# Optimization experiments

Measured on AMD Instinct MI355X. Metric: run time of the kernel, lower is better.

Reference implementation:

```python
import jax, jax.numpy as jnp
import numpy as np

B, T, F, H = 32, 8192, 256, 128


def setup_inputs() -> dict:
    key = jax.random.key(0)
    k1, k2, k3, k4, k5 = jax.random.split(key, 5)
    return {
        "encoder_outputs": jax.random.normal(k1, (B, T, F), dtype=jnp.float32),
        "dec_output": jax.random.normal(k2, (B, F), dtype=jnp.float32),
        "W1": jax.random.normal(k3, (F, H), dtype=jnp.float32) * 0.05,
        "W2": jax.random.normal(k4, (F, H), dtype=jnp.float32) * 0.05,
        "V": jax.random.normal(k5, (H, 1), dtype=jnp.float32) * 0.05,
    }


def reference(encoder_outputs, dec_output, W1, W2, V):
    # w1_e: [B,T,H]; w2_d: [B,1,H] (constant across timesteps, no real recurrence)
    w1_e = jnp.einsum("btf,fh->bth", encoder_outputs, W1)
    w2_d = (dec_output @ W2)[:, None, :]
    # scores[b,t] = V . tanh(W1 e_t + W2 d)  -> [B, T] (raw logits, no softmax in original call)
    scores = jnp.einsum("bth,h->bt", jnp.tanh(w1_e + w2_d), V[:, 0])
    return scores
```

## Files before the change

kernel.cpp:

```cpp
#include <hip/hip_runtime.h>

#define B_ 32
#define T_ 8192
#define F_ 256
#define H_ 128

typedef short bf16x8 __attribute__((ext_vector_type(8)));
typedef float f32x4  __attribute__((ext_vector_type(4)));

static __device__ __forceinline__ unsigned int pack_bf2(float lo, float hi) {
    unsigned int r;
    asm("v_cvt_pk_bf16_f32 %0, %1, %2" : "=v"(r) : "v"(lo), "v"(hi));
    return r;
}

static __device__ __forceinline__ float fast_tanh(float x) {
    float e = __builtin_amdgcn_exp2f(x * 2.8853900817779268f);
    return 1.f - 2.f * __builtin_amdgcn_rcpf(e + 1.f);
}

__global__ __launch_bounds__(256) void prep_kernel(const float* __restrict__ dec,
                                                   const float* __restrict__ W1,
                                                   const float* __restrict__ W2,
                                                   float* __restrict__ w2d,
                                                   uint4* __restrict__ frags) {
    const int blk = blockIdx.x, tid = threadIdx.x;
    if (blk < 32) {
        if (tid < H_) {
            const float* dp = dec + blk * F_;
            float s = 0.f;
            #pragma unroll 8
            for (int f = 0; f < F_; ++f) s += dp[f] * W2[f * H_ + tid];
            w2d[blk * H_ + tid] = s;
        }
    } else {
        const int e = (blk - 32) * 256 + tid;
        const int lane = e & 63;
        const int ks   = (e >> 6) & 7;
        const int nt   = e >> 9;
        const int q = lane >> 4, c = lane & 15;
        const int h = nt * 16 + c;
        const float* src = W1 + (q * 64 + ks * 8) * H_ + h;
        unsigned int u[4];
        #pragma unroll
        for (int jj = 0; jj < 4; ++jj) {
            float a = src[(2 * jj) * H_];
            float b = src[(2 * jj + 1) * H_];
            u[jj] = pack_bf2(a, b);
        }
        frags[e] = uint4{u[0], u[1], u[2], u[3]};
    }
}

__global__ __launch_bounds__(256) void attn_main(const float* __restrict__ enc,
                                                 const float* __restrict__ Vvec,
                                                 const float* __restrict__ w2d,
                                                 const uint4* __restrict__ frags,
                                                 float* __restrict__ out) {
    __shared__ __align__(16) unsigned char tile_lds[2][32 * 512];
    __shared__ float red[4][256];

    const int tid  = threadIdx.x;
    const int blk  = blockIdx.x;
    const int b    = blk >> 5;
    const int t0   = (blk & 31) << 8;
    const int w    = tid >> 6;
    const int lane = tid & 63;
    const int q    = lane >> 4;
    const int c    = lane & 15;

    bf16x8 bw[2][8];
    #pragma unroll
    for (int ntl = 0; ntl < 2; ++ntl)
        #pragma unroll
        for (int ks = 0; ks < 8; ++ks) {
            uint4 u = frags[((2 * w + ntl) * 8 + ks) * 64 + lane];
            bw[ntl][ks] = __builtin_bit_cast(bf16x8, u);
        }

    float Vv[2], wd[2];
    #pragma unroll
    for (int ntl = 0; ntl < 2; ++ntl) {
        const int h = 16 * (2 * w + ntl) + c;
        Vv[ntl] = Vvec[h];
        wd[ntl] = w2d[b * H_ + h];
    }

    const f32x4* src = (const f32x4*)(enc + ((size_t)b * T_ + t0) * F_);
    const int sw = c & 7;

    f32x4 x[8];
    #pragma unroll
    for (int i = 0; i < 8; ++i) x[i] = src[i * 256 + tid];

    for (int ht = 0; ht < 8; ++ht) {
        const int cur = ht & 1;
        unsigned char* buf = tile_lds[cur];

        #pragma unroll
        for (int i = 0; i < 8; ++i) {
            const int flat4 = i * 256 + tid;
            const int row   = flat4 >> 6;
            const int c4    = flat4 & 63;
            const int chunk = (c4 >> 1) ^ (row & 7);
            uint2 v;
            v.x = pack_bf2(x[i][0], x[i][1]);
            v.y = pack_bf2(x[i][2], x[i][3]);
            *(uint2*)(buf + row * 512 + chunk * 16 + (c4 & 1) * 8) = v;
        }

        if (ht < 7) {
            const f32x4* sp = src + (ht + 1) * 2048;
            #pragma unroll
            for (int i = 0; i < 8; ++i) x[i] = sp[i * 256 + tid];
        }

        __syncthreads();

        #pragma unroll
        for (int g = 0; g < 2; ++g) {
            const unsigned char* rbase = buf + (g * 16 + c) * 512;
            f32x4 acc0 = {0.f, 0.f, 0.f, 0.f};
            f32x4 acc1 = {0.f, 0.f, 0.f, 0.f};
            #pragma unroll
            for (int ks = 0; ks < 8; ++ks) {
                bf16x8 a = *(const bf16x8*)(rbase + ((8 * q + ks) ^ sw) * 16);
                acc0 = __builtin_amdgcn_mfma_f32_16x16x32_bf16(a, bw[0][ks], acc0, 0, 0, 0);
                acc1 = __builtin_amdgcn_mfma_f32_16x16x32_bf16(a, bw[1][ks], acc1, 0, 0, 0);
            }
            f32x4 part;
            #pragma unroll
            for (int r = 0; r < 4; ++r)
                part[r] = Vv[0] * fast_tanh(acc0[r] + wd[0])
                        + Vv[1] * fast_tanh(acc1[r] + wd[1]);
            #pragma unroll
            for (int m = 1; m < 16; m <<= 1) {
                #pragma unroll
                for (int r = 0; r < 4; ++r) part[r] += __shfl_xor(part[r], m, 64);
            }
            if (c == 0)
                *(f32x4*)&red[w][ht * 32 + g * 16 + 4 * q] = part;
        }
    }

    __syncthreads();
    {
        float s = red[0][tid] + red[1][tid] + red[2][tid] + red[3][tid];
        out[(size_t)b * T_ + t0 + tid] = s;
    }
}

extern "C" void kernel_launch(void* const* d_in, const int* in_sizes, int n_in,
                              void* d_out, int out_size, void* d_ws, size_t ws_size,
                              hipStream_t stream) {
    const float* enc = (const float*)d_in[0];
    const float* dec = (const float*)d_in[1];
    const float* W1  = (const float*)d_in[2];
    const float* W2  = (const float*)d_in[3];
    const float* V   = (const float*)d_in[4];
    float* out = (float*)d_out;

    float* w2d   = (float*)d_ws;
    uint4* frags = (uint4*)((char*)d_ws + 16384);

    prep_kernel<<<48, 256, 0, stream>>>(dec, W1, W2, w2d, frags);
    attn_main<<<1024, 256, 0, stream>>>(enc, V, w2d, frags, out);
}
```

Measured before the change: 59.80 us.

## Fuse weight prep into main kernel with 512-thread blocks over 512 timesteps

Removes the separate prep kernel: each block now converts its own W1 column slice to bf16 MFMA fragments and computes the W2·dec bias in shared memory. Blocks grow to 8 waves covering 512 timesteps, so each wave handles one 16-column H tile instead of two, with half the register-staged input per thread. The __syncthreads before the MFMA loop is replaced by an explicit lgkmcnt wait plus barrier, which does not wait on the global prefetch loads. The aim is to drop a kernel launch and its dependency gap. In exchange every block redundantly recomputes the W1 conversion and the W2 dot product, using strided global loads.

```diff
diff --git a/kernel.cpp b/kernel.cpp
--- a/kernel.cpp
+++ b/kernel.cpp
@@ -19,87 +19,69 @@
     return 1.f - 2.f * __builtin_amdgcn_rcpf(e + 1.f);
 }
 
-__global__ __launch_bounds__(256) void prep_kernel(const float* __restrict__ dec,
-                                                   const float* __restrict__ W1,
-                                                   const float* __restrict__ W2,
-                                                   float* __restrict__ w2d,
-                                                   uint4* __restrict__ frags) {
-    const int blk = blockIdx.x, tid = threadIdx.x;
-    if (blk < 32) {
-        if (tid < H_) {
-            const float* dp = dec + blk * F_;
-            float s = 0.f;
-            #pragma unroll 8
-            for (int f = 0; f < F_; ++f) s += dp[f] * W2[f * H_ + tid];
-            w2d[blk * H_ + tid] = s;
-        }
-    } else {
-        const int e = (blk - 32) * 256 + tid;
-        const int lane = e & 63;
-        const int ks   = (e >> 6) & 7;
-        const int nt   = e >> 9;
-        const int q = lane >> 4, c = lane & 15;
-        const int h = nt * 16 + c;
-        const float* src = W1 + (q * 64 + ks * 8) * H_ + h;
-        unsigned int u[4];
-        #pragma unroll
-        for (int jj = 0; jj < 4; ++jj) {
-            float a = src[(2 * jj) * H_];
-            float b = src[(2 * jj + 1) * H_];
-            u[jj] = pack_bf2(a, b);
-        }
-        frags[e] = uint4{u[0], u[1], u[2], u[3]};
-    }
-}
-
-__global__ __launch_bounds__(256) void attn_main(const float* __restrict__ enc,
-                                                 const float* __restrict__ Vvec,
-                                                 const float* __restrict__ w2d,
-                                                 const uint4* __restrict__ frags,
-                                                 float* __restrict__ out) {
+__global__ __launch_bounds__(512) void attn_fused(const float* __restrict__ enc,
+                                                  const float* __restrict__ dec,
+                                                  const float* __restrict__ W1,
+                                                  const float* __restrict__ W2,
+                                                  const float* __restrict__ Vvec,
+                                                  float* __restrict__ out) {
     __shared__ __align__(16) unsigned char tile_lds[2][32 * 512];
-    __shared__ float red[4][256];
+    __shared__ float red[8][512];
+    __shared__ float w2dp[4][128];
+    __shared__ float w2dv[128];
 
     const int tid  = threadIdx.x;
     const int blk  = blockIdx.x;
-    const int b    = blk >> 5;
-    const int t0   = (blk & 31) << 8;
+    const int b    = blk >> 4;
+    const int t0   = (blk & 15) << 9;
     const int w    = tid >> 6;
     const int lane = tid & 63;
     const int q    = lane >> 4;
     const int c    = lane & 15;
 
-    bf16x8 bw[2][8];
+    const f32x4* src = (const f32x4*)(enc + ((size_t)b * T_ + t0) * F_);
+
+    f32x4 x[4];
     #pragma unroll
-    for (int ntl = 0; ntl < 2; ++ntl)
+    for (int i = 0; i < 4; ++i) x[i] = src[i * 512 + tid];
+
+    const int h = 16 * w + c;
+    bf16x8 bw[8];
+    #pragma unroll
+    for (int ks = 0; ks < 8; ++ks) {
+        const float* wp = W1 + (64 * q + 8 * ks) * H_ + h;
+        union { bf16x8 v; unsigned int u[4]; } pk;
         #pragma unroll
-        for (int ks = 0; ks < 8; ++ks) {
-            uint4 u = frags[((2 * w + ntl) * 8 + ks) * 64 + lane];
-            bw[ntl][ks] = __builtin_bit_cast(bf16x8, u);
-        }
-
-    float Vv[2], wd[2];
-    #pragma unroll
-    for (int ntl = 0; ntl < 2; ++ntl) {
-        const int h = 16 * (2 * w + ntl) + c;
-        Vv[ntl] = Vvec[h];
-        wd[ntl] = w2d[b * H_ + h];
+        for (int jj = 0; jj < 4; ++jj)
+            pk.u[jj] = pack_bf2(wp[(2 * jj) * H_], wp[(2 * jj + 1) * H_]);
+        bw[ks] = pk.v;
     }
 
-    const f32x4* src = (const f32x4*)(enc + ((size_t)b * T_ + t0) * F_);
+    {
+        const int hh = tid & 127, p = tid >> 7;
+        const float* dp  = dec + b * F_ + p * 64;
+        const float* w2p = W2 + (p * 64) * H_ + hh;
+        float s = 0.f;
+        #pragma unroll 8
+        for (int f = 0; f < 64; ++f) s += dp[f] * w2p[f * H_];
+        w2dp[p][hh] = s;
+    }
+    __syncthreads();
+    if (tid < 128)
+        w2dv[tid] = w2dp[0][tid] + w2dp[1][tid] + w2dp[2][tid] + w2dp[3][tid];
+    __syncthreads();
+
+    const float Vv = Vvec[h];
+    const float wd = w2dv[h];
     const int sw = c & 7;
 
-    f32x4 x[8];
-    #pragma unroll
-    for (int i = 0; i < 8; ++i) x[i] = src[i * 256 + tid];
-
-    for (int ht = 0; ht < 8; ++ht) {
-        const int cur = ht & 1;
-        unsigned char* buf = tile_lds[cur];
+    #pragma unroll 2
+    for (int ht = 0; ht < 16; ++ht) {
+        unsigned char* buf = tile_lds[ht & 1];
 
         #pragma unroll
-        for (int i = 0; i < 8; ++i) {
-            const int flat4 = i * 256 + tid;
+        for (int i = 0; i < 4; ++i) {
+            const int flat4 = i * 512 + tid;
             const int row   = flat4 >> 6;
             const int c4    = flat4 & 63;
             const int chunk = (c4 >> 1) ^ (row & 7);
@@ -109,30 +91,27 @@
             *(uint2*)(buf + row * 512 + chunk * 16 + (c4 & 1) * 8) = v;
         }
 
-        if (ht < 7) {
+        if (ht < 15) {
             const f32x4* sp = src + (ht + 1) * 2048;
             #pragma unroll
-            for (int i = 0; i < 8; ++i) x[i] = sp[i * 256 + tid];
+            for (int i = 0; i < 4; ++i) x[i] = sp[i * 512 + tid];
         }
 
-        __syncthreads();
+        asm volatile("s_waitcnt lgkmcnt(0)\n\ts_barrier" ::: "memory");
 
         #pragma unroll
         for (int g = 0; g < 2; ++g) {
             const unsigned char* rbase = buf + (g * 16 + c) * 512;
-            f32x4 acc0 = {0.f, 0.f, 0.f, 0.f};
-            f32x4 acc1 = {0.f, 0.f, 0.f, 0.f};
+            f32x4 acc = {0.f, 0.f, 0.f, 0.f};
             #pragma unroll
             for (int ks = 0; ks < 8; ++ks) {
                 bf16x8 a = *(const bf16x8*)(rbase + ((8 * q + ks) ^ sw) * 16);
-                acc0 = __builtin_amdgcn_mfma_f32_16x16x32_bf16(a, bw[0][ks], acc0, 0, 0, 0);
-                acc1 = __builtin_amdgcn_mfma_f32_16x16x32_bf16(a, bw[1][ks], acc1, 0, 0, 0);
+                acc = __builtin_amdgcn_mfma_f32_16x16x32_bf16(a, bw[ks], acc, 0, 0, 0);
             }
             f32x4 part;
             #pragma unroll
             for (int r = 0; r < 4; ++r)
-                part[r] = Vv[0] * fast_tanh(acc0[r] + wd[0])
-                        + Vv[1] * fast_tanh(acc1[r] + wd[1]);
+                part[r] = Vv * fast_tanh(acc[r] + wd);
             #pragma unroll
             for (int m = 1; m < 16; m <<= 1) {
                 #pragma unroll
@@ -144,10 +123,10 @@
     }
 
     __syncthreads();
-    {
-        float s = red[0][tid] + red[1][tid] + red[2][tid] + red[3][tid];
-        out[(size_t)b * T_ + t0 + tid] = s;
-    }
+    float s = 0.f;
+    #pragma unroll
+    for (int ww = 0; ww < 8; ++ww) s += red[ww][tid];
+    out[(size_t)b * T_ + t0 + tid] = s;
 }
 
 extern "C" void kernel_launch(void* const* d_in, const int* in_sizes, int n_in,
@@ -160,9 +139,5 @@
     const float* V   = (const float*)d_in[4];
     float* out = (float*)d_out;
 
-    float* w2d   = (float*)d_ws;
-    uint4* frags = (uint4*)((char*)d_ws + 16384);
-
-    prep_kernel<<<48, 256, 0, stream>>>(dec, W1, W2, w2d, frags);
-    attn_main<<<1024, 256, 0, stream>>>(enc, V, w2d, frags, out);
+    attn_fused<<<512, 512, 0, stream>>>(enc, dec, W1, W2, V, out);
 }
```

Result: faster. 53.85 us (-9.9%).
